# Kernel optimization log

Measured on AMD Instinct MI355X. Metric: run time of the kernel, lower is better.

The kernel has to match this reference:

```python
import jax, jax.numpy as jnp
import numpy as np

DIM = 64        # feature channels of x
HEADS = 4
POS_DIM = 3
NUM_IDS = 8
STR_IN = 512    # strength_linear input size
B, S, W = 4, 1024, 8   # batch, sequence (S1), source-views (S2)


def setup_inputs() -> dict:
    key = jax.random.key(0)
    ks = jax.random.split(key, 18)
    stdv = 1.0 / np.sqrt(DIM * DIM)  # embedding init per module
    d8 = DIM // 8
    u = lambda k, shp, s: jax.random.uniform(k, shp, jnp.float32, -s, s)
    return {
        "x": jax.random.normal(ks[0], (B, DIM, S, W), jnp.float32),
        "pos": jax.random.normal(ks[1], (B, S, POS_DIM), jnp.float32),
        "strength": jax.random.normal(ks[2], (STR_IN,), jnp.float32),
        "embed_id1": 3,
        "q_emb_w": u(ks[3], (NUM_IDS, DIM * DIM), stdv),
        "k_emb_w": u(ks[4], (NUM_IDS, DIM * DIM), stdv),
        "v_emb_w": u(ks[5], (NUM_IDS, DIM * DIM), stdv),
        "pos_w1": u(ks[6], (POS_DIM, POS_DIM), 1.0 / np.sqrt(POS_DIM)),
        "pos_b1": u(ks[7], (POS_DIM,), 1.0 / np.sqrt(POS_DIM)),
        "pos_w2": u(ks[8], (d8, POS_DIM), 1.0 / np.sqrt(POS_DIM)),
        "pos_b2": u(ks[9], (d8,), 1.0 / np.sqrt(POS_DIM)),
        "head_w": u(ks[10], (HEADS, d8), 1.0 / np.sqrt(d8)),
        "head_b": u(ks[11], (HEADS,), 1.0 / np.sqrt(d8)),
        "gate": jnp.ones((HEADS,), jnp.float32),
        "out_w": u(ks[12], (DIM, DIM), 1.0 / np.sqrt(DIM)),
        "out_b": u(ks[13], (DIM,), 1.0 / np.sqrt(DIM)),
        "str_w": u(ks[14], (DIM, STR_IN), 1.0 / np.sqrt(STR_IN)),
        "str_b": u(ks[15], (DIM,), 1.0 / np.sqrt(STR_IN)),
    }


def reference(x, pos, strength, embed_id1, q_emb_w, k_emb_w, v_emb_w,
              pos_w1, pos_b1, pos_w2, pos_b2, head_w, head_b, gate,
              out_w, out_b, str_w, str_b):
    # strength projection: Linear(512, dim)
    s = strength @ str_w.T + str_b                    # [dim]
    xt = jnp.transpose(x, (0, 2, 3, 1))               # [B, S, W, dim]
    qe = q_emb_w[embed_id1].reshape(DIM, DIM)
    ke = k_emb_w[embed_id1].reshape(DIM, DIM)
    ve = v_emb_w[embed_id1].reshape(DIM, DIM)

    def proj(emb):
        y = xt @ emb.T + s                            # [B, S, W, dim]
        # collapse (W, dim) -> (heads, head_dim), heads to axis 1
        y = y.reshape(B, S, HEADS, -1)
        return jnp.transpose(y, (0, 2, 1, 3))         # [B, H, S, hd]

    q, k, v = proj(qe), proj(ke), proj(ve)
    hd = q.shape[-1]
    attn = jax.nn.softmax(jnp.einsum("bhsd,bhtd->bhst", q, k) / np.sqrt(hd), axis=-1)

    # relative-position attention branch
    ph = jax.nn.relu(pos @ pos_w1.T + pos_b1) @ pos_w2.T + pos_b2   # [B, S, dim//8]
    diff = ph[:, :, None, :] - ph[:, None, :, :]                    # [B, S, S, dim//8]
    pos_attn = jnp.transpose(diff @ head_w.T + head_b, (0, 3, 1, 2))
    pos_attn = jax.nn.softmax(pos_attn, axis=-1)                    # [B, H, S, S]

    g = jax.nn.sigmoid(gate).reshape(1, -1, 1, 1)
    attn = (1.0 - g) * attn + g * pos_attn
    attn = attn / jnp.sum(attn, axis=-1, keepdims=True)

    out = jnp.einsum("bhst,bhtd->bhsd", attn, v)      # [B, H, S, hd]
    out = jnp.transpose(out, (0, 2, 1, 3)).reshape(B, S, W, DIM)
    return out @ out_w.T + out_b                      # [B, S, W, dim]
```

## Files before the change

### kernel.cpp

```cpp
#include <hip/hip_runtime.h>
#include <math.h>
#include <stdint.h>

#define B_ 4
#define S_ 1024
#define F_ 512
#define HD 128
#define SOFT_C 4.0f

typedef __attribute__((ext_vector_type(8))) short short8;
typedef __attribute__((ext_vector_type(4))) float f32x4;
typedef __attribute__((ext_vector_type(4))) unsigned int u32x4;
typedef __attribute__((ext_vector_type(2))) unsigned int u32x2;

__device__ __forceinline__ unsigned short f2bf(float f) {
    unsigned int u = __float_as_uint(f);
    u = (u + 0x7FFFu + ((u >> 16) & 1u)) >> 16;
    return (unsigned short)u;
}
__device__ __forceinline__ float bf2f(unsigned int s) {
    return __uint_as_float(s << 16);
}
__device__ __forceinline__ void pack_hilo(const float* v, u32x4& hi, u32x4& lo) {
    #pragma unroll
    for (int p = 0; p < 4; ++p) {
        unsigned int h0 = f2bf(v[2 * p]), h1 = f2bf(v[2 * p + 1]);
        float l0 = v[2 * p] - bf2f(h0), l1 = v[2 * p + 1] - bf2f(h1);
        hi[p] = h0 | (h1 << 16);
        lo[p] = (unsigned int)f2bf(l0) | ((unsigned int)f2bf(l1) << 16);
    }
}

__global__ __launch_bounds__(256) void k_prep(
    const int* __restrict__ embed_id,
    const float* __restrict__ qw, const float* __restrict__ kw,
    const float* __restrict__ vw, const float* __restrict__ ow,
    const float* __restrict__ pos,
    const float* __restrict__ pw1, const float* __restrict__ pb1,
    const float* __restrict__ pw2, const float* __restrict__ pb2,
    const float* __restrict__ head_w,
    const float* __restrict__ strength, const float* __restrict__ str_w,
    const float* __restrict__ str_b,
    unsigned short* __restrict__ packs,
    float* __restrict__ sv, float* __restrict__ svq,
    float* __restrict__ p_g)
{
    __shared__ float red_s[4][4];
    __shared__ float inv_s[4];
    const int blk = blockIdx.x, tid = threadIdx.x;
    const float SCALE = 0.08838834764831845f;

    if (blk < 4) {
        const int id = embed_id[0];
        const float* src = (blk == 0 ? qw + id * 4096 : blk == 1 ? kw + id * 4096
                            : blk == 2 ? vw + id * 4096 : ow);
        const float scale = (blk == 0) ? SCALE : 1.0f;
        unsigned short* hi = packs + blk * 8192;
        unsigned short* lo = hi + 4096;
        for (int i = tid; i < 4096; i += 256) {
            float v = src[i] * scale;
            unsigned short h = f2bf(v);
            hi[i] = h;
            lo[i] = f2bf(v - bf2f(h));
        }
    } else if (blk < 8) {
        const int b = blk - 4;
        const int wv = tid >> 6;
        float w1_[9], b1_[3], w2_[24], b2_[8], hw_[32];
        #pragma unroll
        for (int i = 0; i < 9; ++i)  w1_[i] = pw1[i];
        #pragma unroll
        for (int i = 0; i < 3; ++i)  b1_[i] = pb1[i];
        #pragma unroll
        for (int i = 0; i < 24; ++i) w2_[i] = pw2[i];
        #pragma unroll
        for (int i = 0; i < 8; ++i)  b2_[i] = pb2[i];
        #pragma unroll
        for (int i = 0; i < 32; ++i) hw_[i] = head_w[i];

        float ev[4][4];
        float ps[4] = {0.f, 0.f, 0.f, 0.f};
        #pragma unroll
        for (int k = 0; k < 4; ++k) {
            const int t = k * 256 + tid;
            float p0 = pos[(b * S_ + t) * 3 + 0];
            float p1 = pos[(b * S_ + t) * 3 + 1];
            float p2 = pos[(b * S_ + t) * 3 + 2];
            float h0 = fmaxf(0.f, p0 * w1_[0] + p1 * w1_[1] + p2 * w1_[2] + b1_[0]);
            float h1 = fmaxf(0.f, p0 * w1_[3] + p1 * w1_[4] + p2 * w1_[5] + b1_[1]);
            float h2 = fmaxf(0.f, p0 * w1_[6] + p1 * w1_[7] + p2 * w1_[8] + b1_[2]);
            float ph[8];
            #pragma unroll
            for (int o8 = 0; o8 < 8; ++o8)
                ph[o8] = h0 * w2_[o8 * 3] + h1 * w2_[o8 * 3 + 1] + h2 * w2_[o8 * 3 + 2] + b2_[o8];
            #pragma unroll
            for (int h = 0; h < 4; ++h) {
                float A = 0.f;
                #pragma unroll
                for (int o8 = 0; o8 < 8; ++o8) A += ph[o8] * hw_[h * 8 + o8];
                ev[k][h] = __expf(-A - 1.0f);
                ps[h] += ev[k][h];
            }
        }
        #pragma unroll
        for (int h = 0; h < 4; ++h)
            #pragma unroll
            for (int off = 1; off < 64; off <<= 1)
                ps[h] += __shfl_xor(ps[h], off);
        if ((tid & 63) == 0)
            #pragma unroll
            for (int h = 0; h < 4; ++h) red_s[wv][h] = ps[h];
        __syncthreads();
        if (tid < 4)
            inv_s[tid] = 1.f / (red_s[0][tid] + red_s[1][tid] + red_s[2][tid] + red_s[3][tid]);
        __syncthreads();
        #pragma unroll
        for (int k = 0; k < 4; ++k)
            #pragma unroll
            for (int h = 0; h < 4; ++h)
                p_g[(b * 4 + h) * S_ + k * 256 + tid] = ev[k][h] * inv_s[h];
    } else {
        __shared__ float part_s[4][64];
        const int c = tid & 63, pr = tid >> 6;
        const float* wrow = str_w + c * 512 + pr * 128;
        const float* st   = strength + pr * 128;
        float acc = 0.f;
        #pragma unroll
        for (int j4 = 0; j4 < 32; ++j4) {
            f32x4 wv4 = *(const f32x4*)(wrow + j4 * 4);
            f32x4 s4  = *(const f32x4*)(st + j4 * 4);
            acc += wv4[0] * s4[0] + wv4[1] * s4[1] + wv4[2] * s4[2] + wv4[3] * s4[3];
        }
        part_s[pr][c] = acc;
        __syncthreads();
        if (tid < 64) {
            float v = part_s[0][tid] + part_s[1][tid] + part_s[2][tid]
                    + part_s[3][tid] + str_b[tid];
            sv[tid] = v;
            svq[tid] = v * SCALE;
        }
    }
}

__global__ __launch_bounds__(256) void k_qkv(
    const float* __restrict__ x,
    const unsigned short* __restrict__ packs,
    const float* __restrict__ sv, const float* __restrict__ svq,
    const float* __restrict__ p_g,
    unsigned short* __restrict__ yqh, unsigned short* __restrict__ ykh,
    unsigned short* __restrict__ yvt2, float* __restrict__ xbar)
{
    __shared__ float xr_s[4][8];
    const int tid  = threadIdx.x;
    const int wv   = tid >> 6;
    const int lane = tid & 63;
    const int quad = lane >> 4;
    const int l15  = lane & 15;

    if (blockIdx.x >= 512) {
        const int bi = blockIdx.x - 512;
        const int b = bi >> 6, c = bi & 63;
        const float* xc = x + (size_t)b * 524288 + c * 8192;
        const float* pb = p_g + b * 4096;
        float acc[8] = {};
        #pragma unroll
        for (int rr = 0; rr < 4; ++rr) {
            const int s = tid * 4 + rr;
            f32x4 x0 = *(const f32x4*)(xc + s * 8);
            f32x4 x1 = *(const f32x4*)(xc + s * 8 + 4);
            float p0 = pb[s], p1 = pb[1024 + s], p2 = pb[2048 + s], p3 = pb[3072 + s];
            acc[0] += p0 * x0[0]; acc[1] += p0 * x0[1];
            acc[2] += p1 * x0[2]; acc[3] += p1 * x0[3];
            acc[4] += p2 * x1[0]; acc[5] += p2 * x1[1];
            acc[6] += p3 * x1[2]; acc[7] += p3 * x1[3];
        }
        #pragma unroll
        for (int j = 0; j < 8; ++j)
            #pragma unroll
            for (int off = 1; off < 64; off <<= 1)
                acc[j] += __shfl_xor(acc[j], off);
        if (lane == 0)
            #pragma unroll
            for (int j = 0; j < 8; ++j) xr_s[wv][j] = acc[j];
        __syncthreads();
        if (tid < 8)
            xbar[(b * 8 + tid) * 64 + c] = xr_s[0][tid] + xr_s[1][tid]
                                         + xr_s[2][tid] + xr_s[3][tid];
        return;
    }

    const int r0   = blockIdx.x * 64 + wv * 16;
    const int b    = r0 >> 13;
    const int rloc = (r0 & 8191) + l15;
    const float* xb = x + (size_t)b * 524288;

    u32x4 xhi[2], xlo[2];
    #pragma unroll
    for (int kc = 0; kc < 2; ++kc) {
        float xv[8];
        #pragma unroll
        for (int j = 0; j < 8; ++j)
            xv[j] = xb[(kc * 32 + quad * 8 + j) * 8192 + rloc];
        pack_hilo(xv, xhi[kc], xlo[kc]);
    }

    float svq_l[4], sv_l[4];
    #pragma unroll
    for (int nt = 0; nt < 4; ++nt) {
        svq_l[nt] = svq[nt * 16 + l15];
        sv_l[nt]  = sv[nt * 16 + l15];
    }
    f32x4 svA[4];
    #pragma unroll
    for (int mt = 0; mt < 4; ++mt)
        svA[mt] = *(const f32x4*)(sv + mt * 16 + quad * 4);

    int idxq[4];
    #pragma unroll
    for (int rr = 0; rr < 4; ++rr) {
        const int rl = quad * 4 + rr;
        const int w_ = rl & 7;
        const int s_loc = ((r0 & 8191) >> 3) + (rl >> 3);
        idxq[rr] = (b * 4 + (w_ >> 1)) * 131072 + s_loc * 128 + (w_ & 1) * 64 + l15;
    }

    const int row_g = r0 + l15;
    const int s_idx = (row_g >> 3) & 1023;
    const int w_idx = row_g & 7;
    const int bh    = b * 4 + (w_idx >> 1);
    const int dbase = (w_idx & 1) * 64;
    unsigned short* vtb = yvt2 + (size_t)bh * 131072 + (s_idx >> 6) * 8192
                        + (size_t)dbase * 64 + (s_idx & 63);

    #pragma unroll
    for (int mat = 0; mat < 2; ++mat) {
        const unsigned short* mh = packs + mat * 8192;
        const unsigned short* ml = mh + 4096;
        f32x4 acc[4] = {};
        #pragma unroll
        for (int kc = 0; kc < 2; ++kc)
            #pragma unroll
            for (int nt = 0; nt < 4; ++nt) {
                const int off = (nt * 16 + l15) * 64 + kc * 32 + quad * 8;
                u32x4 ehi = *(const u32x4*)(mh + off);
                u32x4 elo = *(const u32x4*)(ml + off);
                acc[nt] = __builtin_amdgcn_mfma_f32_16x16x32_bf16(
                    __builtin_bit_cast(short8, xhi[kc]),
                    __builtin_bit_cast(short8, ehi), acc[nt], 0, 0, 0);
                acc[nt] = __builtin_amdgcn_mfma_f32_16x16x32_bf16(
                    __builtin_bit_cast(short8, xlo[kc]),
                    __builtin_bit_cast(short8, ehi), acc[nt], 0, 0, 0);
                acc[nt] = __builtin_amdgcn_mfma_f32_16x16x32_bf16(
                    __builtin_bit_cast(short8, xhi[kc]),
                    __builtin_bit_cast(short8, elo), acc[nt], 0, 0, 0);
            }
        unsigned short* y = (mat == 0 ? yqh : ykh);
        const float* svp = (mat == 0 ? svq_l : sv_l);
        #pragma unroll
        for (int nt = 0; nt < 4; ++nt)
            #pragma unroll
            for (int rr = 0; rr < 4; ++rr)
                y[(size_t)idxq[rr] + nt * 16] = f2bf(acc[nt][rr] + svp[nt]);
    }

    {
        const unsigned short* mh = packs + 2 * 8192;
        const unsigned short* ml = mh + 4096;
        f32x4 acc[4] = {};
        #pragma unroll
        for (int kc = 0; kc < 2; ++kc)
            #pragma unroll
            for (int mt = 0; mt < 4; ++mt) {
                const int off = (mt * 16 + l15) * 64 + kc * 32 + quad * 8;
                u32x4 ehi = *(const u32x4*)(mh + off);
                u32x4 elo = *(const u32x4*)(ml + off);
                acc[mt] = __builtin_amdgcn_mfma_f32_16x16x32_bf16(
                    __builtin_bit_cast(short8, ehi),
                    __builtin_bit_cast(short8, xhi[kc]), acc[mt], 0, 0, 0);
                acc[mt] = __builtin_amdgcn_mfma_f32_16x16x32_bf16(
                    __builtin_bit_cast(short8, ehi),
                    __builtin_bit_cast(short8, xlo[kc]), acc[mt], 0, 0, 0);
                acc[mt] = __builtin_amdgcn_mfma_f32_16x16x32_bf16(
                    __builtin_bit_cast(short8, elo),
                    __builtin_bit_cast(short8, xhi[kc]), acc[mt], 0, 0, 0);
            }
        #pragma unroll
        for (int mt = 0; mt < 4; ++mt)
            #pragma unroll
            for (int rr = 0; rr < 4; ++rr) {
                const int c = mt * 16 + quad * 4 + rr;
                vtb[(size_t)c * 64] = f2bf(acc[mt][rr] + svA[mt][rr]);
            }
    }
}

__global__ __launch_bounds__(256, 2) void k_attn(
    const unsigned short* __restrict__ yqh, const unsigned short* __restrict__ ykh,
    const unsigned short* __restrict__ yvt2,
    const float* __restrict__ xbar, const float* __restrict__ vw,
    const int* __restrict__ embed_id, const float* __restrict__ sv,
    const float* __restrict__ gate, float* __restrict__ out)
{
    __shared__ __align__(16) unsigned short kx[2][64 * 136];
    __shared__ __align__(16) unsigned short vx[2][128 * 72];
    __shared__ float vbar_s[128];

    const int tid  = threadIdx.x;
    const int w    = tid >> 6;
    const int lane = tid & 63;
    const int quad = lane >> 4;
    const int l15  = lane & 15;
    const int bh = blockIdx.x & 15, qt = blockIdx.x >> 4;
    const int b = bh >> 2, h = bh & 3;
    const int s0 = qt * 32;
    const int qh = w >> 1;
    const int dh = w & 1;

    const unsigned short* ykb = ykh + (size_t)bh * 131072;
    const unsigned short* yvb = yvt2 + (size_t)bh * 131072;

    if (tid < 128) {
        const int c = tid & 63, wloc = tid >> 6;
        const float* ver = vw + embed_id[0] * 4096 + c * 64;
        const float* xbr = xbar + (b * 8 + h * 2 + wloc) * 64;
        float a = sv[c];
        #pragma unroll
        for (int j4 = 0; j4 < 16; ++j4) {
            f32x4 e4 = *(const f32x4*)(ver + j4 * 4);
            f32x4 x4 = *(const f32x4*)(xbr + j4 * 4);
            a += e4[0] * x4[0] + e4[1] * x4[1] + e4[2] * x4[2] + e4[3] * x4[3];
        }
        vbar_s[wloc * 64 + c] = a;
    }

    u32x4 qf[4];
    #pragma unroll
    for (int kc = 0; kc < 4; ++kc)
        qf[kc] = *(const u32x4*)(yqh + (size_t)bh * 131072
                 + (s0 + qh * 16 + l15) * 128 + kc * 32 + quad * 8);

    #pragma unroll
    for (int r = 0; r < 4; ++r) {
        const int off = r * 2048 + tid * 8;
        *(u32x4*)&kx[0][(off >> 7) * 136 + (off & 127)] =
            *(const u32x4*)(ykb + off);
        *(u32x4*)&vx[0][(off >> 6) * 72 + (off & 63)] =
            *(const u32x4*)(yvb + off);
    }
    __syncthreads();

    f32x4 o[4] = {};
    float lsum = 0.f;
    const int srcA = ((quad & 1) << 5) + l15;

    for (int it = 0; it < 16; ++it) {
        const int cur = it & 1;
        u32x4 kst[4], vst[4];
        const bool pre = (it < 15);
        if (pre) {
            const unsigned short* ksrc = ykb + (it + 1) * 8192;
            const unsigned short* vsrc = yvb + (it + 1) * 8192;
            #pragma unroll
            for (int r = 0; r < 4; ++r)
                kst[r] = *(const u32x4*)(ksrc + r * 2048 + tid * 8);
            #pragma unroll
            for (int r = 0; r < 4; ++r)
                vst[r] = *(const u32x4*)(vsrc + r * 2048 + tid * 8);
        }

        const unsigned short* kxc = kx[cur];
        const unsigned short* vxc = vx[cur];

        #pragma unroll
        for (int th = 0; th < 2; ++th) {
            f32x4 sa0 = {}, sa1 = {};
            #pragma unroll
            for (int kc = 0; kc < 4; ++kc) {
                u32x4 a0 = *(const u32x4*)&kxc[(th * 32 + l15) * 136 + kc * 32 + quad * 8];
                sa0 = __builtin_amdgcn_mfma_f32_16x16x32_bf16(
                    __builtin_bit_cast(short8, a0),
                    __builtin_bit_cast(short8, qf[kc]), sa0, 0, 0, 0);
            }
            #pragma unroll
            for (int kc = 0; kc < 4; ++kc) {
                u32x4 a1 = *(const u32x4*)&kxc[(th * 32 + 16 + l15) * 136 + kc * 32 + quad * 8];
                sa1 = __builtin_amdgcn_mfma_f32_16x16x32_bf16(
                    __builtin_bit_cast(short8, a1),
                    __builtin_bit_cast(short8, qf[kc]), sa1, 0, 0, 0);
            }

            float p0[4], p1[4];
            #pragma unroll
            for (int r = 0; r < 4; ++r) {
                p0[r] = __expf(sa0[r] - SOFT_C);
                p1[r] = __expf(sa1[r] - SOFT_C);
                lsum += p0[r] + p1[r];
            }

            unsigned int pk00 = (unsigned int)f2bf(p0[0]) | ((unsigned int)f2bf(p0[1]) << 16);
            unsigned int pk01 = (unsigned int)f2bf(p0[2]) | ((unsigned int)f2bf(p0[3]) << 16);
            unsigned int pk10 = (unsigned int)f2bf(p1[0]) | ((unsigned int)f2bf(p1[1]) << 16);
            unsigned int pk11 = (unsigned int)f2bf(p1[2]) | ((unsigned int)f2bf(p1[3]) << 16);
            unsigned int sel0 = (quad < 2) ? pk00 : pk10;
            unsigned int sel1 = (quad < 2) ? pk01 : pk11;
            u32x4 pf;
            pf[0] = (unsigned int)__shfl((int)sel0, srcA);
            pf[1] = (unsigned int)__shfl((int)sel1, srcA);
            pf[2] = (unsigned int)__shfl((int)sel0, srcA + 16);
            pf[3] = (unsigned int)__shfl((int)sel1, srcA + 16);

            #pragma unroll
            for (int dt = 0; dt < 4; ++dt) {
                u32x4 vf = *(const u32x4*)&vxc[(dh * 64 + dt * 16 + l15) * 72
                                               + th * 32 + quad * 8];
                o[dt] = __builtin_amdgcn_mfma_f32_16x16x32_bf16(
                    __builtin_bit_cast(short8, vf),
                    __builtin_bit_cast(short8, pf), o[dt], 0, 0, 0);
            }
        }

        if (pre) {
            #pragma unroll
            for (int r = 0; r < 4; ++r) {
                const int off = r * 2048 + tid * 8;
                *(u32x4*)&kx[cur ^ 1][(off >> 7) * 136 + (off & 127)] = kst[r];
            }
            #pragma unroll
            for (int r = 0; r < 4; ++r) {
                const int off = r * 2048 + tid * 8;
                *(u32x4*)&vx[cur ^ 1][(off >> 6) * 72 + (off & 63)] = vst[r];
            }
        }
        __syncthreads();
    }

    lsum += __shfl_xor(lsum, 16);
    lsum += __shfl_xor(lsum, 32);
    const float gf = 1.f / (1.f + __expf(-gate[h]));
    const float cf = (1.f - gf) / lsum;
    const int row = b * S_ + s0 + qh * 16 + l15;
    #pragma unroll
    for (int dt = 0; dt < 4; ++dt) {
        const int d0 = dh * 64 + dt * 16 + quad * 4;
        f32x4 vb = *(const f32x4*)&vbar_s[d0];
        f32x4 rv;
        #pragma unroll
        for (int j = 0; j < 4; ++j) rv[j] = cf * o[dt][j] + gf * vb[j];
        *(f32x4*)(out + (size_t)row * F_ + h * HD + d0) = rv;
    }
}

__global__ __launch_bounds__(256) void k_oproj(
    float* __restrict__ out, const unsigned short* __restrict__ packs,
    const float* __restrict__ ob)
{
    const int tid  = threadIdx.x;
    const int wv   = tid >> 6;
    const int lane = tid & 63;
    const int quad = lane >> 4;
    const int l15  = lane & 15;
    const int r0   = blockIdx.x * 64 + wv * 16;
    const unsigned short* owh = packs + 3 * 8192;
    const unsigned short* owl = owh + 4096;

    u32x4 bhi[2], blo[2];
    #pragma unroll
    for (int kc = 0; kc < 2; ++kc) {
        const float* src = out + (size_t)(r0 + l15) * 64 + kc * 32 + quad * 8;
        f32x4 y0 = *(const f32x4*)src;
        f32x4 y1 = *(const f32x4*)(src + 4);
        float yv8[8] = {y0[0], y0[1], y0[2], y0[3], y1[0], y1[1], y1[2], y1[3]};
        pack_hilo(yv8, bhi[kc], blo[kc]);
    }

    f32x4 acc[4] = {};
    #pragma unroll
    for (int kc = 0; kc < 2; ++kc)
        #pragma unroll
        for (int mt = 0; mt < 4; ++mt) {
            const int off = (mt * 16 + l15) * 64 + kc * 32 + quad * 8;
            u32x4 ahi = *(const u32x4*)(owh + off);
            u32x4 alo = *(const u32x4*)(owl + off);
            acc[mt] = __builtin_amdgcn_mfma_f32_16x16x32_bf16(
                __builtin_bit_cast(short8, ahi),
                __builtin_bit_cast(short8, bhi[kc]), acc[mt], 0, 0, 0);
            acc[mt] = __builtin_amdgcn_mfma_f32_16x16x32_bf16(
                __builtin_bit_cast(short8, ahi),
                __builtin_bit_cast(short8, blo[kc]), acc[mt], 0, 0, 0);
            acc[mt] = __builtin_amdgcn_mfma_f32_16x16x32_bf16(
                __builtin_bit_cast(short8, alo),
                __builtin_bit_cast(short8, bhi[kc]), acc[mt], 0, 0, 0);
        }

    #pragma unroll
    for (int mt = 0; mt < 4; ++mt) {
        f32x4 bias = *(const f32x4*)(ob + mt * 16 + quad * 4);
        f32x4 v = acc[mt] + bias;
        *(f32x4*)(out + (size_t)(r0 + l15) * 64 + mt * 16 + quad * 4) = v;
    }
}

extern "C" void kernel_launch(void* const* d_in, const int* in_sizes, int n_in,
                              void* d_out, int out_size, void* d_ws, size_t ws_size,
                              hipStream_t stream) {
    (void)in_sizes; (void)n_in; (void)out_size; (void)ws_size;
    const float* x        = (const float*)d_in[0];
    const float* pos      = (const float*)d_in[1];
    const float* strength = (const float*)d_in[2];
    const int*   embed_id = (const int*)d_in[3];
    const float* qw       = (const float*)d_in[4];
    const float* kw       = (const float*)d_in[5];
    const float* vw       = (const float*)d_in[6];
    const float* pw1      = (const float*)d_in[7];
    const float* pb1      = (const float*)d_in[8];
    const float* pw2      = (const float*)d_in[9];
    const float* pb2      = (const float*)d_in[10];
    const float* head_w   = (const float*)d_in[11];
    const float* gate     = (const float*)d_in[13];
    const float* out_w    = (const float*)d_in[14];
    const float* out_b    = (const float*)d_in[15];
    const float* str_w    = (const float*)d_in[16];
    const float* str_b    = (const float*)d_in[17];
    float* out = (float*)d_out;

    unsigned short* yqh   = (unsigned short*)d_ws;
    unsigned short* ykh   = yqh + 2097152;
    unsigned short* yvt2  = ykh + 2097152;
    unsigned short* packs = yvt2 + 2097152;
    float* sv   = (float*)(packs + 8 * 4096);
    float* svq  = sv + 64;
    float* p_g  = svq + 64;
    float* xbar = p_g + 16384;

    k_prep<<<9, 256, 0, stream>>>(embed_id, qw, kw, vw, out_w, pos,
                                  pw1, pb1, pw2, pb2, head_w,
                                  strength, str_w, str_b, packs, sv, svq, p_g);
    k_qkv<<<768, 256, 0, stream>>>(x, packs, sv, svq, p_g, yqh, ykh, yvt2, xbar);
    k_attn<<<512, 256, 0, stream>>>(yqh, ykh, yvt2, xbar, vw, embed_id, sv,
                                    gate, out);
    k_oproj<<<512, 256, 0, stream>>>(out, packs, out_b);
}
```

Measured before the change: 157.1 us.

## Fuse output projection into attention kernel and split key range across waves

The separate output-projection kernel is removed and its matmul is folded into the attention epilogue. The gated mean-V term is pre-projected through out_w and combined with the bias per block. Each block now handles 16 query rows instead of 32, with the two wave pairs splitting each 64-key tile and reducing their partials through LDS. Blocks double to 1024, LDS shrinks from double to single buffering, and the launch-bounds occupancy hint goes from 2 to 4. This drops one kernel launch and a full round trip of the intermediate through global memory, at the cost of an extra barrier per iteration and a cross-wave reduction.

Result: slower. 165.5 us (+5.4%).

```diff
diff --git a/kernel.cpp b/kernel.cpp
--- a/kernel.cpp
+++ b/kernel.cpp
@@ -223,7 +223,6 @@
         const int s_loc = ((r0 & 8191) >> 3) + (rl >> 3);
         idxq[rr] = (b * 4 + (w_ >> 1)) * 131072 + s_loc * 128 + (w_ & 1) * 64 + l15;
     }
-
     const int row_g = r0 + l15;
     const int s_idx = (row_g >> 3) & 1023;
     const int w_idx = row_g & 7;
@@ -262,7 +261,6 @@
             for (int rr = 0; rr < 4; ++rr)
                 y[(size_t)idxq[rr] + nt * 16] = f2bf(acc[nt][rr] + svp[nt]);
     }
-
     {
         const unsigned short* mh = packs + 2 * 8192;
         const unsigned short* ml = mh + 4096;
@@ -294,16 +292,21 @@
     }
 }
 
-__global__ __launch_bounds__(256, 2) void k_attn(
+__global__ __launch_bounds__(256, 4) void k_attn(
     const unsigned short* __restrict__ yqh, const unsigned short* __restrict__ ykh,
     const unsigned short* __restrict__ yvt2,
     const float* __restrict__ xbar, const float* __restrict__ vw,
-    const int* __restrict__ embed_id, const float* __restrict__ sv,
-    const float* __restrict__ gate, float* __restrict__ out)
+    const int* __restrict__ embed_id, const float* __restrict__ sv_g,
+    const float* __restrict__ gate,
+    const unsigned short* __restrict__ packs,
+    const float* __restrict__ ow, const float* __restrict__ ob,
+    float* __restrict__ out)
 {
-    __shared__ __align__(16) unsigned short kx[2][64 * 136];
-    __shared__ __align__(16) unsigned short vx[2][128 * 72];
+    __shared__ __align__(16) unsigned short kx[64 * 136];
+    __shared__ __align__(16) unsigned short vx[128 * 72];
     __shared__ float vbar_s[128];
+    __shared__ float vproj_s[128];
+    __shared__ float lsh[2][16];
 
     const int tid  = threadIdx.x;
     const int w    = tid >> 6;
@@ -312,18 +315,19 @@
     const int l15  = lane & 15;
     const int bh = blockIdx.x & 15, qt = blockIdx.x >> 4;
     const int b = bh >> 2, h = bh & 3;
-    const int s0 = qt * 32;
-    const int qh = w >> 1;
+    const int s0 = qt * 16;
+    const int th = w >> 1;
     const int dh = w & 1;
 
     const unsigned short* ykb = ykh + (size_t)bh * 131072;
     const unsigned short* yvb = yvt2 + (size_t)bh * 131072;
+    const float gf = 1.f / (1.f + __expf(-gate[h]));
 
     if (tid < 128) {
         const int c = tid & 63, wloc = tid >> 6;
         const float* ver = vw + embed_id[0] * 4096 + c * 64;
         const float* xbr = xbar + (b * 8 + h * 2 + wloc) * 64;
-        float a = sv[c];
+        float a = sv_g[c];
         #pragma unroll
         for (int j4 = 0; j4 < 16; ++j4) {
             f32x4 e4 = *(const f32x4*)(ver + j4 * 4);
@@ -337,27 +341,44 @@
     #pragma unroll
     for (int kc = 0; kc < 4; ++kc)
         qf[kc] = *(const u32x4*)(yqh + (size_t)bh * 131072
-                 + (s0 + qh * 16 + l15) * 128 + kc * 32 + quad * 8);
-
+                 + (s0 + l15) * 128 + kc * 32 + quad * 8);
+
+    u32x4 kst[4], vst[4];
     #pragma unroll
     for (int r = 0; r < 4; ++r) {
-        const int off = r * 2048 + tid * 8;
-        *(u32x4*)&kx[0][(off >> 7) * 136 + (off & 127)] =
-            *(const u32x4*)(ykb + off);
-        *(u32x4*)&vx[0][(off >> 6) * 72 + (off & 63)] =
-            *(const u32x4*)(yvb + off);
-    }
+        kst[r] = *(const u32x4*)(ykb + r * 2048 + tid * 8);
+        vst[r] = *(const u32x4*)(yvb + r * 2048 + tid * 8);
+    }
+
     __syncthreads();
+    if (tid < 128) {
+        const int cp = tid & 63, w2 = tid >> 6;
+        const float* owr = ow + cp * 64;
+        const float* vb = vbar_s + w2 * 64;
+        float a = 0.f;
+        #pragma unroll
+        for (int j4 = 0; j4 < 16; ++j4) {
+            f32x4 o4 = *(const f32x4*)(owr + j4 * 4);
+            f32x4 v4 = *(const f32x4*)(vb + j4 * 4);
+            a += o4[0] * v4[0] + o4[1] * v4[1] + o4[2] * v4[2] + o4[3] * v4[3];
+        }
+        vproj_s[tid] = gf * a + ob[cp];
+    }
 
     f32x4 o[4] = {};
     float lsum = 0.f;
     const int srcA = ((quad & 1) << 5) + l15;
+    const int t0loc = th * 32;
 
     for (int it = 0; it < 16; ++it) {
-        const int cur = it & 1;
-        u32x4 kst[4], vst[4];
-        const bool pre = (it < 15);
-        if (pre) {
+        #pragma unroll
+        for (int r = 0; r < 4; ++r) {
+            const int off = r * 2048 + tid * 8;
+            *(u32x4*)&kx[(off >> 7) * 136 + (off & 127)] = kst[r];
+            *(u32x4*)&vx[(off >> 6) * 72 + (off & 63)] = vst[r];
+        }
+        __syncthreads();
+        if (it < 15) {
             const unsigned short* ksrc = ykb + (it + 1) * 8192;
             const unsigned short* vsrc = yvb + (it + 1) * 8192;
             #pragma unroll
@@ -368,135 +389,126 @@
                 vst[r] = *(const u32x4*)(vsrc + r * 2048 + tid * 8);
         }
 
-        const unsigned short* kxc = kx[cur];
-        const unsigned short* vxc = vx[cur];
-
-        #pragma unroll
-        for (int th = 0; th < 2; ++th) {
-            f32x4 sa0 = {}, sa1 = {};
-            #pragma unroll
-            for (int kc = 0; kc < 4; ++kc) {
-                u32x4 a0 = *(const u32x4*)&kxc[(th * 32 + l15) * 136 + kc * 32 + quad * 8];
-                sa0 = __builtin_amdgcn_mfma_f32_16x16x32_bf16(
-                    __builtin_bit_cast(short8, a0),
-                    __builtin_bit_cast(short8, qf[kc]), sa0, 0, 0, 0);
-            }
-            #pragma unroll
-            for (int kc = 0; kc < 4; ++kc) {
-                u32x4 a1 = *(const u32x4*)&kxc[(th * 32 + 16 + l15) * 136 + kc * 32 + quad * 8];
-                sa1 = __builtin_amdgcn_mfma_f32_16x16x32_bf16(
-                    __builtin_bit_cast(short8, a1),
-                    __builtin_bit_cast(short8, qf[kc]), sa1, 0, 0, 0);
-            }
-
-            float p0[4], p1[4];
-            #pragma unroll
-            for (int r = 0; r < 4; ++r) {
-                p0[r] = __expf(sa0[r] - SOFT_C);
-                p1[r] = __expf(sa1[r] - SOFT_C);
-                lsum += p0[r] + p1[r];
-            }
-
-            unsigned int pk00 = (unsigned int)f2bf(p0[0]) | ((unsigned int)f2bf(p0[1]) << 16);
-            unsigned int pk01 = (unsigned int)f2bf(p0[2]) | ((unsigned int)f2bf(p0[3]) << 16);
-            unsigned int pk10 = (unsigned int)f2bf(p1[0]) | ((unsigned int)f2bf(p1[1]) << 16);
-            unsigned int pk11 = (unsigned int)f2bf(p1[2]) | ((unsigned int)f2bf(p1[3]) << 16);
-            unsigned int sel0 = (quad < 2) ? pk00 : pk10;
-            unsigned int sel1 = (quad < 2) ? pk01 : pk11;
-            u32x4 pf;
-            pf[0] = (unsigned int)__shfl((int)sel0, srcA);
-            pf[1] = (unsigned int)__shfl((int)sel1, srcA);
-            pf[2] = (unsigned int)__shfl((int)sel0, srcA + 16);
-            pf[3] = (unsigned int)__shfl((int)sel1, srcA + 16);
-
-            #pragma unroll
-            for (int dt = 0; dt < 4; ++dt) {
-                u32x4 vf = *(const u32x4*)&vxc[(dh * 64 + dt * 16 + l15) * 72
-                                               + th * 32 + quad * 8];
-                o[dt] = __builtin_amdgcn_mfma_f32_16x16x32_bf16(
-                    __builtin_bit_cast(short8, vf),
-                    __builtin_bit_cast(short8, pf), o[dt], 0, 0, 0);
-            }
-        }
-
-        if (pre) {
-            #pragma unroll
-            for (int r = 0; r < 4; ++r) {
-                const int off = r * 2048 + tid * 8;
-                *(u32x4*)&kx[cur ^ 1][(off >> 7) * 136 + (off & 127)] = kst[r];
-            }
-            #pragma unroll
-            for (int r = 0; r < 4; ++r) {
-                const int off = r * 2048 + tid * 8;
-                *(u32x4*)&vx[cur ^ 1][(off >> 6) * 72 + (off & 63)] = vst[r];
-            }
+        f32x4 sa0 = {}, sa1 = {};
+        #pragma unroll
+        for (int kc = 0; kc < 4; ++kc) {
+            u32x4 a0 = *(const u32x4*)&kx[(t0loc + l15) * 136 + kc * 32 + quad * 8];
+            sa0 = __builtin_amdgcn_mfma_f32_16x16x32_bf16(
+                __builtin_bit_cast(short8, a0),
+                __builtin_bit_cast(short8, qf[kc]), sa0, 0, 0, 0);
+        }
+        #pragma unroll
+        for (int kc = 0; kc < 4; ++kc) {
+            u32x4 a1 = *(const u32x4*)&kx[(t0loc + 16 + l15) * 136 + kc * 32 + quad * 8];
+            sa1 = __builtin_amdgcn_mfma_f32_16x16x32_bf16(
+                __builtin_bit_cast(short8, a1),
+                __builtin_bit_cast(short8, qf[kc]), sa1, 0, 0, 0);
+        }
+
+        float p0[4], p1[4];
+        #pragma unroll
+        for (int r = 0; r < 4; ++r) {
+            p0[r] = __expf(sa0[r] - SOFT_C);
+            p1[r] = __expf(sa1[r] - SOFT_C);
+            lsum += p0[r] + p1[r];
+        }
+
+        unsigned int pk00 = (unsigned int)f2bf(p0[0]) | ((unsigned int)f2bf(p0[1]) << 16);
+        unsigned int pk01 = (unsigned int)f2bf(p0[2]) | ((unsigned int)f2bf(p0[3]) << 16);
+        unsigned int pk10 = (unsigned int)f2bf(p1[0]) | ((unsigned int)f2bf(p1[1]) << 16);
+        unsigned int pk11 = (unsigned int)f2bf(p1[2]) | ((unsigned int)f2bf(p1[3]) << 16);
+        unsigned int sel0 = (quad < 2) ? pk00 : pk10;
+        unsigned int sel1 = (quad < 2) ? pk01 : pk11;
+        u32x4 pf;
+        pf[0] = (unsigned int)__shfl((int)sel0, srcA);
+        pf[1] = (unsigned int)__shfl((int)sel1, srcA);
+        pf[2] = (unsigned int)__shfl((int)sel0, srcA + 16);
+        pf[3] = (unsigned int)__shfl((int)sel1, srcA + 16);
+
+        #pragma unroll
+        for (int dt = 0; dt < 4; ++dt) {
+            u32x4 vf = *(const u32x4*)&vx[(dh * 64 + dt * 16 + l15) * 72
+                                           + t0loc + quad * 8];
+            o[dt] = __builtin_amdgcn_mfma_f32_16x16x32_bf16(
+                __builtin_bit_cast(short8, vf),
+                __builtin_bit_cast(short8, pf), o[dt], 0, 0, 0);
         }
         __syncthreads();
     }
 
     lsum += __shfl_xor(lsum, 16);
     lsum += __shfl_xor(lsum, 32);
-    const float gf = 1.f / (1.f + __expf(-gate[h]));
-    const float cf = (1.f - gf) / lsum;
-    const int row = b * S_ + s0 + qh * 16 + l15;
-    #pragma unroll
-    for (int dt = 0; dt < 4; ++dt) {
-        const int d0 = dh * 64 + dt * 16 + quad * 4;
-        f32x4 vb = *(const f32x4*)&vbar_s[d0];
-        f32x4 rv;
-        #pragma unroll
-        for (int j = 0; j < 4; ++j) rv[j] = cf * o[dt][j] + gf * vb[j];
-        *(f32x4*)(out + (size_t)row * F_ + h * HD + d0) = rv;
-    }
-}
-
-__global__ __launch_bounds__(256) void k_oproj(
-    float* __restrict__ out, const unsigned short* __restrict__ packs,
-    const float* __restrict__ ob)
-{
-    const int tid  = threadIdx.x;
-    const int wv   = tid >> 6;
-    const int lane = tid & 63;
-    const int quad = lane >> 4;
-    const int l15  = lane & 15;
-    const int r0   = blockIdx.x * 64 + wv * 16;
-    const unsigned short* owh = packs + 3 * 8192;
-    const unsigned short* owl = owh + 4096;
-
-    u32x4 bhi[2], blo[2];
-    #pragma unroll
-    for (int kc = 0; kc < 2; ++kc) {
-        const float* src = out + (size_t)(r0 + l15) * 64 + kc * 32 + quad * 8;
-        f32x4 y0 = *(const f32x4*)src;
-        f32x4 y1 = *(const f32x4*)(src + 4);
-        float yv8[8] = {y0[0], y0[1], y0[2], y0[3], y1[0], y1[1], y1[2], y1[3]};
-        pack_hilo(yv8, bhi[kc], blo[kc]);
-    }
-
-    f32x4 acc[4] = {};
-    #pragma unroll
-    for (int kc = 0; kc < 2; ++kc)
+    float* cmb = (float*)kx;
+    if (th == 1) {
+        #pragma unroll
+        for (int dt = 0; dt < 4; ++dt)
+            *(f32x4*)&cmb[(dh * 16 + l15) * 68 + dt * 16 + quad * 4] = o[dt];
+        if (quad == 0) lsh[dh][l15] = lsum;
+    }
+    __syncthreads();
+    if (th == 0) {
+        #pragma unroll
+        for (int dt = 0; dt < 4; ++dt) {
+            f32x4 p = *(const f32x4*)&cmb[(dh * 16 + l15) * 68 + dt * 16 + quad * 4];
+            o[dt] += p;
+        }
+        lsum += lsh[dh][l15];
+        const float cf = (1.f - gf) / lsum;
+
+        unsigned short* yst = (unsigned short*)vx + dh * 4352;
+        #pragma unroll
+        for (int dt = 0; dt < 4; ++dt) {
+            unsigned int hh[4];
+            unsigned short ll[4];
+            #pragma unroll
+            for (int r = 0; r < 4; ++r) {
+                float y = cf * o[dt][r];
+                hh[r] = f2bf(y);
+                ll[r] = f2bf(y - bf2f(hh[r]));
+            }
+            const int dloc = dt * 16 + quad * 4;
+            u32x2 ph_, pl_;
+            ph_[0] = hh[0] | (hh[1] << 16);
+            ph_[1] = hh[2] | (hh[3] << 16);
+            pl_[0] = (unsigned int)ll[0] | ((unsigned int)ll[1] << 16);
+            pl_[1] = (unsigned int)ll[2] | ((unsigned int)ll[3] << 16);
+            *(u32x2*)&yst[l15 * 68 + dloc] = ph_;
+            *(u32x2*)&yst[1088 + l15 * 68 + dloc] = pl_;
+        }
+        u32x4 ybh[2], ybl[2];
+        #pragma unroll
+        for (int kc = 0; kc < 2; ++kc) {
+            ybh[kc] = *(const u32x4*)&yst[l15 * 68 + kc * 32 + quad * 8];
+            ybl[kc] = *(const u32x4*)&yst[1088 + l15 * 68 + kc * 32 + quad * 8];
+        }
+        const unsigned short* owh = packs + 3 * 8192;
+        const unsigned short* owl = owh + 4096;
+        f32x4 accp[4] = {};
+        #pragma unroll
+        for (int kc = 0; kc < 2; ++kc)
+            #pragma unroll
+            for (int mt = 0; mt < 4; ++mt) {
+                const int off = (mt * 16 + l15) * 64 + kc * 32 + quad * 8;
+                u32x4 ahi = *(const u32x4*)(owh + off);
+                u32x4 alo = *(const u32x4*)(owl + off);
+                accp[mt] = __builtin_amdgcn_mfma_f32_16x16x32_bf16(
+                    __builtin_bit_cast(short8, ahi),
+                    __builtin_bit_cast(short8, ybh[kc]), accp[mt], 0, 0, 0);
+                accp[mt] = __builtin_amdgcn_mfma_f32_16x16x32_bf16(
+                    __builtin_bit_cast(short8, ahi),
+                    __builtin_bit_cast(short8, ybl[kc]), accp[mt], 0, 0, 0);
+                accp[mt] = __builtin_amdgcn_mfma_f32_16x16x32_bf16(
+                    __builtin_bit_cast(short8, alo),
+                    __builtin_bit_cast(short8, ybh[kc]), accp[mt], 0, 0, 0);
+            }
+        const int sQ = s0 + l15;
+        float* op = out + ((size_t)((b * S_ + sQ) * 8 + 2 * h + dh)) * 64;
         #pragma unroll
         for (int mt = 0; mt < 4; ++mt) {
-            const int off = (mt * 16 + l15) * 64 + kc * 32 + quad * 8;
-            u32x4 ahi = *(const u32x4*)(owh + off);
-            u32x4 alo = *(const u32x4*)(owl + off);
-            acc[mt] = __builtin_amdgcn_mfma_f32_16x16x32_bf16(
-                __builtin_bit_cast(short8, ahi),
-                __builtin_bit_cast(short8, bhi[kc]), acc[mt], 0, 0, 0);
-            acc[mt] = __builtin_amdgcn_mfma_f32_16x16x32_bf16(
-                __builtin_bit_cast(short8, ahi),
-                __builtin_bit_cast(short8, blo[kc]), acc[mt], 0, 0, 0);
-            acc[mt] = __builtin_amdgcn_mfma_f32_16x16x32_bf16(
-                __builtin_bit_cast(short8, alo),
-                __builtin_bit_cast(short8, bhi[kc]), acc[mt], 0, 0, 0);
-        }
-
-    #pragma unroll
-    for (int mt = 0; mt < 4; ++mt) {
-        f32x4 bias = *(const f32x4*)(ob + mt * 16 + quad * 4);
-        f32x4 v = acc[mt] + bias;
-        *(f32x4*)(out + (size_t)(r0 + l15) * 64 + mt * 16 + quad * 4) = v;
+            f32x4 vp = *(const f32x4*)&vproj_s[dh * 64 + mt * 16 + quad * 4];
+            f32x4 rv = accp[mt] + vp;
+            *(f32x4*)(op + mt * 16 + quad * 4) = rv;
+        }
     }
 }
 
@@ -536,7 +548,6 @@
                                   pw1, pb1, pw2, pb2, head_w,
                                   strength, str_w, str_b, packs, sv, svq, p_g);
     k_qkv<<<768, 256, 0, stream>>>(x, packs, sv, svq, p_g, yqh, ykh, yvt2, xbar);
-    k_attn<<<512, 256, 0, stream>>>(yqh, ykh, yvt2, xbar, vw, embed_id, sv,
-                                    gate, out);
-    k_oproj<<<512, 256, 0, stream>>>(out, packs, out_b);
-}
+    k_attn<<<1024, 256, 0, stream>>>(yqh, ykh, yvt2, xbar, vw, embed_id, sv,
+                                     gate, packs, out_w, out_b, out);
+}
```
